# Optimization experiments

Hardware: AMD Instinct MI355X
Metric: run time of the kernel (lower is better)

Reference implementation:

```python
import jax, jax.numpy as jnp
import numpy as np

N_NODES = 100000
N_EDGES = 1600000
D = 32
K = 3  # Chebyshev kernels
NEG_SLOPE = 0.2


def setup_inputs() -> dict:
    key = jax.random.key(0)
    ks = jax.random.split(key, 10)
    s = 1.0 / np.sqrt(D)
    return {
        "u": jax.random.normal(ks[0], (N_NODES, D), jnp.float32),
        "lambda_max": jnp.full((1,), 2.0, jnp.float32),
        "edge_src": jax.random.randint(ks[1], (N_EDGES,), 0, N_NODES, jnp.int32),
        "edge_dst": jax.random.randint(ks[2], (N_EDGES,), 0, N_NODES, jnp.int32),
        "cheb_W": jax.random.normal(ks[3], (K * D, D), jnp.float32) * s,
        "cheb_b": jnp.zeros((D,), jnp.float32),
        "src_W": jax.random.normal(ks[4], (D, D), jnp.float32) * s,
        "src_b": jnp.zeros((D,), jnp.float32),
        "dst_W": jax.random.normal(ks[5], (D, D), jnp.float32) * s,
        "dst_b": jnp.zeros((D,), jnp.float32),
        "attn": jax.random.normal(ks[6], (1, D), jnp.float32) * s,  # (heads=1, D)
    }


def reference(u, lambda_max, edge_src, edge_dst, cheb_W, cheb_b,
              src_W, src_b, dst_W, dst_b, attn):
    N = u.shape[0]
    # in-degrees (DGL: clamp(min=1) ** -0.5)
    deg = jnp.zeros((N,), u.dtype).at[edge_dst].add(1.0)
    Dinv = jnp.clip(deg, 1.0, None) ** -0.5  # (N,)

    def unnL(x):  # D^{-1/2} A D^{-1/2} x  via copy_u->sum message passing
        m = (x * Dinv[:, None])[edge_src]                       # (E, D)
        agg = jax.ops.segment_sum(m, edge_dst, num_segments=N)  # (N, D)
        return agg * Dinv[:, None]

    # --- ChebConv ---
    re_norm = 2.0 / lambda_max  # (1,) broadcast over all nodes
    X0 = u
    Xt = [X0]
    X1 = X0
    if K > 1:
        h = unnL(X0)
        X1 = -re_norm * h + X0 * (re_norm - 1.0)
        Xt.append(X1)
    for _ in range(2, K):
        h = unnL(X1)
        Xi = -2.0 * re_norm * h + X1 * (2.0 * (re_norm - 1.0)) - X0
        Xt.append(Xi)
        X0, X1 = X1, Xi
    Xcat = jnp.concatenate(Xt, axis=1)                 # (N, K*D)
    hc = jax.nn.relu(Xcat @ cheb_W + cheb_b)           # (N, D), DGL default activation=relu

    # --- GATv2Conv (heads=1) ---
    H = attn.shape[0]
    fsrc = (hc @ src_W + src_b).reshape(N, H, -1)      # (N, H, D)
    fdst = (hc @ dst_W + dst_b).reshape(N, H, -1)
    e = jax.nn.leaky_relu(fsrc[edge_src] + fdst[edge_dst], NEG_SLOPE)  # (E, H, D)
    logits = jnp.einsum('ehd,hd->eh', e, attn)         # (E, H)
    mx = jax.ops.segment_max(logits, edge_dst, num_segments=N)
    mx = jnp.where(jnp.isfinite(mx), mx, 0.0)
    ex = jnp.exp(logits - mx[edge_dst])
    den = jax.ops.segment_sum(ex, edge_dst, num_segments=N)
    a = ex / jnp.where(den > 0, den, 1.0)[edge_dst]    # edge softmax over dst groups
    msg = fsrc[edge_src] * a[:, :, None]               # (E, H, D)
    out = jax.ops.segment_sum(msg, edge_dst, num_segments=N)  # (N, H, D)
    return out.squeeze(1)
```

## Files before the change

kernel.cpp:

```cpp
#include <hip/hip_runtime.h>
#include <hip/hip_bf16.h>


typedef unsigned short u16;

#define DD 32
#define NEG_SLOPE 0.2f
#define BLK 256
#define TILE 4096
#define CB_SHIFT 8
#define CB_NODES 256
#define SRC_BITS 17

#define OFF_CHEBW 0
#define OFF_CHEBB 3072
#define OFF_SRCW  3104
#define OFF_SRCB  4128
#define OFF_DSTW  4160
#define OFF_DSTB  5184
#define OFF_ATTN  5216
#define OFF_LMAX  5248
#define W_TOTAL   5249

#define F_U     0
#define F_CHEBW 1
#define F_CHEBB 2
#define F_SRCW  3
#define F_SRCB  4
#define F_DSTW  5
#define F_DSTB  6
#define F_ATTN  7
#define F_LMAX  8
#define N_FLAGS 9

__device__ __forceinline__ float bh2f(u16 h) {
    return __uint_as_float(((unsigned)h) << 16);
}
__device__ __forceinline__ float rdin(const void* p, long long i, int f32f) {
    return f32f ? ((const float*)p)[i] : bh2f(((const u16*)p)[i]);
}
__device__ __forceinline__ float4 rd4(const void* p, long long row, int q, int f32f) {
    if (f32f) return ((const float4*)p)[row * 8 + q];
    ushort4 h = ((const ushort4*)p)[row * 8 + q];
    return make_float4(bh2f(h.x), bh2f(h.y), bh2f(h.z), bh2f(h.w));
}
__device__ __forceinline__ float lrelu(float x) { return fmaxf(x, NEG_SLOPE * x); }

__device__ __forceinline__ int plaus(u16 h) {
    if ((h & 0x7FFFu) == 0) return 1;
    unsigned e = (h >> 7) & 0xFF;
    return (e >= 0x60 && e <= 0x8F) ? 1 : 0;
}

__global__ void k_detect(const void* p0, const void* p1, const void* p2,
                         const void* p3, const void* p4, const void* p5,
                         const void* p6, const void* p7, const void* p8,
                         int n0, int n7, int* __restrict__ flags) {
    __shared__ int cEven, cEvenZ, cOddNZ;
    const void* ptrs[N_FLAGS] = {p0, p1, p2, p3, p4, p5, p6, p7, p8};
    const int   ns[N_FLAGS]   = {n0, 3072, 32, 1024, 32, 1024, 32, n7, 1};
    int a = blockIdx.x;
    if (a >= N_FLAGS) return;
    const u16* h = (const u16*)ptrs[a];
    int n = ns[a];
    if (threadIdx.x == 0) { cEven = 0; cEvenZ = 0; cOddNZ = 0; }
    __syncthreads();
    if (n == 1) {
        if (threadIdx.x == 0) {
            u16 v = h[0];
            flags[a] = ((v & 0x7FFFu) == 0 || !plaus(v)) ? 1 : 0;
        }
        return;
    }
    int nprobe = n >> 1;
    if (nprobe > 64) nprobe = 64;
    int t = threadIdx.x;
    if (t < nprobe) {
        u16 ev = h[2 * t];
        u16 od = h[2 * t + 1];
        if (plaus(ev)) atomicAdd(&cEven, 1);
        if ((ev & 0x7FFFu) == 0) atomicAdd(&cEvenZ, 1);
        if (plaus(od) && (od & 0x7FFFu) != 0) atomicAdd(&cOddNZ, 1);
    }
    __syncthreads();
    if (threadIdx.x == 0) {
        int bf = (cEven * 4 >= nprobe * 3);
        if (cEvenZ == nprobe && cOddNZ * 2 >= nprobe) bf = 0;
        flags[a] = bf ? 0 : 1;
    }
}

__global__ void k_cvtw(const void* chebW, const void* chebB, const void* srcW,
                       const void* srcB, const void* dstW, const void* dstB,
                       const void* attn, const void* lmax,
                       const int* __restrict__ flags, float* __restrict__ wsW,
                       unsigned* __restrict__ Mabs) {
    int i = blockIdx.x * blockDim.x + threadIdx.x;
    if (i >= W_TOTAL + 32) return;
    if (i >= W_TOTAL) { Mabs[i - W_TOTAL] = 0u; return; }
    float v;
    if      (i < OFF_CHEBB) v = rdin(chebW, i - OFF_CHEBW, flags[F_CHEBW]);
    else if (i < OFF_SRCW)  v = rdin(chebB, i - OFF_CHEBB, flags[F_CHEBB]);
    else if (i < OFF_SRCB)  v = rdin(srcW,  i - OFF_SRCW,  flags[F_SRCW]);
    else if (i < OFF_DSTW)  v = rdin(srcB,  i - OFF_SRCB,  flags[F_SRCB]);
    else if (i < OFF_DSTB)  v = rdin(dstW,  i - OFF_DSTW,  flags[F_DSTW]);
    else if (i < OFF_ATTN)  v = rdin(dstB,  i - OFF_DSTB,  flags[F_DSTB]);
    else if (i < OFF_LMAX)  v = rdin(attn,  i - OFF_ATTN,  flags[F_ATTN]);
    else                    v = rdin(lmax,  0,             flags[F_LMAX]);
    wsW[i] = v;
}


__global__ __launch_bounds__(BLK) void k_h1(
        const int* __restrict__ dst, unsigned* __restrict__ hist1,
        int E, int T, int NB1) {
    __shared__ unsigned lh[512];
    int tile = blockIdx.x, t = threadIdx.x;
    for (int b = t; b < 512; b += BLK) lh[b] = 0;
    __syncthreads();
    int base = tile * TILE;
    for (int i = 0; i < TILE / BLK; i++) {
        int e = base + i * BLK + t;
        if (e < E) atomicAdd(&lh[dst[e] >> CB_SHIFT], 1u);
    }
    __syncthreads();
    for (int b = t; b < NB1; b += BLK) hist1[(size_t)b * T + tile] = lh[b];
}

__global__ __launch_bounds__(BLK) void k_scA(
        unsigned* __restrict__ h, unsigned* __restrict__ bsum, int T) {
    __shared__ unsigned s[BLK];
    int b = blockIdx.x, t = threadIdx.x;
    unsigned carry = 0;
    for (int base = 0; base < T; base += BLK) {
        int i = base + t;
        unsigned v = (i < T) ? h[(size_t)b * T + i] : 0u;
        s[t] = v;
        __syncthreads();
        for (int off = 1; off < BLK; off <<= 1) {
            unsigned a = (t >= off) ? s[t - off] : 0u;
            __syncthreads();
            s[t] += a;
            __syncthreads();
        }
        if (i < T) h[(size_t)b * T + i] = carry + s[t] - v;
        carry += s[BLK - 1];
        __syncthreads();
    }
    if (t == 0) bsum[b] = carry;
}

__global__ __launch_bounds__(512) void k_scB(
        unsigned* __restrict__ bsum, int NB1,
        unsigned* __restrict__ row_ptr, int N, int E) {
    __shared__ unsigned s[512];
    int t = threadIdx.x;
    unsigned v = (t < NB1) ? bsum[t] : 0u;
    s[t] = v;
    __syncthreads();
    for (int off = 1; off < 512; off <<= 1) {
        unsigned a = (t >= off) ? s[t - off] : 0u;
        __syncthreads();
        s[t] += a;
        __syncthreads();
    }
    if (t < NB1) bsum[t] = s[t] - v;
    if (t == 0) row_ptr[N] = (unsigned)E;
}

__global__ __launch_bounds__(BLK) void k_s1(
        const int* __restrict__ src, const int* __restrict__ dst,
        const unsigned* __restrict__ off1, const unsigned* __restrict__ bsum,
        unsigned* __restrict__ tmp, int E, int T, int NB1) {
    __shared__ unsigned cur[512];
    int tile = blockIdx.x, t = threadIdx.x;
    for (int b = t; b < NB1; b += BLK)
        cur[b] = off1[(size_t)b * T + tile] + bsum[b];
    __syncthreads();
    int base = tile * TILE;
    for (int i = 0; i < TILE / BLK; i++) {
        int e = base + i * BLK + t;
        if (e < E) {
            int d = dst[e];
            unsigned pos = atomicAdd(&cur[d >> CB_SHIFT], 1u);
            tmp[pos] = ((unsigned)(d & (CB_NODES - 1)) << SRC_BITS) | (unsigned)src[e];
        }
    }
}

__global__ __launch_bounds__(BLK) void k_p2(
        const unsigned* __restrict__ tmp, const unsigned* __restrict__ bsum,
        unsigned* __restrict__ row_ptr, float* __restrict__ dinv,
        int* __restrict__ srcs, int N, int E, int T, int NB1) {
    __shared__ unsigned hist[CB_NODES], cur[CB_NODES], ssc[BLK];
    int b = blockIdx.x, t = threadIdx.x;
    int nodeBase = b << CB_SHIFT;
    unsigned lo = bsum[b];
    unsigned hi = (b + 1 < NB1) ? bsum[b + 1] : (unsigned)E;
    hist[t] = 0;
    __syncthreads();
    for (unsigned e = lo + t; e < hi; e += BLK)
        atomicAdd(&hist[tmp[e] >> SRC_BITS], 1u);
    __syncthreads();
    unsigned v = hist[t];
    ssc[t] = v;
    __syncthreads();
    for (int off = 1; off < BLK; off <<= 1) {
        unsigned a = (t >= off) ? ssc[t - off] : 0u;
        __syncthreads();
        ssc[t] += a;
        __syncthreads();
    }
    unsigned ex = ssc[t] - v;
    cur[t] = ex;
    int node = nodeBase + t;
    if (node < N) {
        row_ptr[node] = lo + ex;
        unsigned c = v;
        if (c < 1u) c = 1u;
        dinv[node] = rsqrtf((float)c);
    }
    __syncthreads();
    for (unsigned e = lo + t; e < hi; e += BLK) {
        unsigned p = tmp[e];
        unsigned pos = lo + atomicAdd(&cur[p >> SRC_BITS], 1u);
        srcs[pos] = (int)(p & ((1u << SRC_BITS) - 1u));
    }
}


__global__ __launch_bounds__(BLK) void k_unnl1(
        const void* __restrict__ u, const int* __restrict__ flags,
        const float* __restrict__ dinv, const unsigned* __restrict__ row_ptr,
        const int* __restrict__ srcs, const float* __restrict__ wsW,
        float* __restrict__ X1, int N) {
    int node = (blockIdx.x * BLK + threadIdx.x) >> 3;
    if (node >= N) return;
    int q = threadIdx.x & 7;
    int f = flags[F_U];
    int base = (int)row_ptr[node], end = (int)row_ptr[node + 1];
    float4 acc = make_float4(0.f, 0.f, 0.f, 0.f);
    for (int i = base; i < end; i += 4) {
        int e1 = i + 1, e2 = i + 2, e3 = i + 3;
        int s0 = srcs[i];
        int s1 = srcs[min(e1, end - 1)];
        int s2 = srcs[min(e2, end - 1)];
        int s3 = srcs[min(e3, end - 1)];
        float dv0 = dinv[s0], dv1 = dinv[s1], dv2 = dinv[s2], dv3 = dinv[s3];
        if (e1 >= end) dv1 = 0.f;
        if (e2 >= end) dv2 = 0.f;
        if (e3 >= end) dv3 = 0.f;
        float4 x0 = rd4(u, s0, q, f);
        float4 x1 = rd4(u, s1, q, f);
        float4 x2 = rd4(u, s2, q, f);
        float4 x3 = rd4(u, s3, q, f);
        acc.x += x0.x * dv0 + x1.x * dv1 + x2.x * dv2 + x3.x * dv3;
        acc.y += x0.y * dv0 + x1.y * dv1 + x2.y * dv2 + x3.y * dv3;
        acc.z += x0.z * dv0 + x1.z * dv1 + x2.z * dv2 + x3.z * dv3;
        acc.w += x0.w * dv0 + x1.w * dv1 + x2.w * dv2 + x3.w * dv3;
    }
    float rn = 2.0f / wsW[OFF_LMAX];
    float dn = dinv[node];
    float4 x0 = rd4(u, node, q, f);
    float4 r;
    r.x = -rn * (acc.x * dn) + x0.x * (rn - 1.f);
    r.y = -rn * (acc.y * dn) + x0.y * (rn - 1.f);
    r.z = -rn * (acc.z * dn) + x0.z * (rn - 1.f);
    r.w = -rn * (acc.w * dn) + x0.w * (rn - 1.f);
    ((float4*)X1)[(size_t)node * 8 + q] = r;
}

__global__ __launch_bounds__(BLK) void k_unnl2(
        const void* __restrict__ u, const int* __restrict__ flags,
        const float* __restrict__ X1, const float* __restrict__ dinv,
        const unsigned* __restrict__ row_ptr, const int* __restrict__ srcs,
        const float* __restrict__ wsW, float* __restrict__ X2, int N) {
    int node = (blockIdx.x * BLK + threadIdx.x) >> 3;
    if (node >= N) return;
    int q = threadIdx.x & 7;
    int base = (int)row_ptr[node], end = (int)row_ptr[node + 1];
    float4 acc = make_float4(0.f, 0.f, 0.f, 0.f);
    for (int i = base; i < end; i += 4) {
        int e1 = i + 1, e2 = i + 2, e3 = i + 3;
        int s0 = srcs[i];
        int s1 = srcs[min(e1, end - 1)];
        int s2 = srcs[min(e2, end - 1)];
        int s3 = srcs[min(e3, end - 1)];
        float dv0 = dinv[s0], dv1 = dinv[s1], dv2 = dinv[s2], dv3 = dinv[s3];
        if (e1 >= end) dv1 = 0.f;
        if (e2 >= end) dv2 = 0.f;
        if (e3 >= end) dv3 = 0.f;
        float4 x0 = ((const float4*)X1)[(size_t)s0 * 8 + q];
        float4 x1 = ((const float4*)X1)[(size_t)s1 * 8 + q];
        float4 x2 = ((const float4*)X1)[(size_t)s2 * 8 + q];
        float4 x3 = ((const float4*)X1)[(size_t)s3 * 8 + q];
        acc.x += x0.x * dv0 + x1.x * dv1 + x2.x * dv2 + x3.x * dv3;
        acc.y += x0.y * dv0 + x1.y * dv1 + x2.y * dv2 + x3.y * dv3;
        acc.z += x0.z * dv0 + x1.z * dv1 + x2.z * dv2 + x3.z * dv3;
        acc.w += x0.w * dv0 + x1.w * dv1 + x2.w * dv2 + x3.w * dv3;
    }
    float rn = 2.0f / wsW[OFF_LMAX];
    float dn = dinv[node];
    float4 x0 = rd4(u, node, q, flags[F_U]);
    float4 x1 = ((const float4*)X1)[(size_t)node * 8 + q];
    float4 r;
    r.x = -2.f * rn * (acc.x * dn) + x1.x * (2.f * (rn - 1.f)) - x0.x;
    r.y = -2.f * rn * (acc.y * dn) + x1.y * (2.f * (rn - 1.f)) - x0.y;
    r.z = -2.f * rn * (acc.z * dn) + x1.z * (2.f * (rn - 1.f)) - x0.z;
    r.w = -2.f * rn * (acc.w * dn) + x1.w * (2.f * (rn - 1.f)) - x0.w;
    ((float4*)X2)[(size_t)node * 8 + q] = r;
}

__global__ __launch_bounds__(BLK) void k_cfsd(
        const void* __restrict__ u, const int* __restrict__ flags,
        const float* __restrict__ X1, const float* __restrict__ X2,
        const float* __restrict__ wsW, float* __restrict__ fsrc,
        float* __restrict__ fdst, unsigned* __restrict__ Mabs, int N) {
    __shared__ float sW[3072], sWs[1024], sWd[1024];
    __shared__ float sb[32], sbs[32], sbd[32];
    __shared__ float hcS[BLK * 33];
    __shared__ unsigned mloc[32];
    int t = threadIdx.x;
    for (int i = t; i < 3072; i += BLK) sW[i] = wsW[OFF_CHEBW + i];
    for (int i = t; i < 1024; i += BLK) {
        sWs[i] = wsW[OFF_SRCW + i];
        sWd[i] = wsW[OFF_DSTW + i];
    }
    if (t < 32) {
        sb[t]  = wsW[OFF_CHEBB + t];
        sbs[t] = wsW[OFF_SRCB + t];
        sbd[t] = wsW[OFF_DSTB + t];
        mloc[t] = 0u;
    }
    __syncthreads();
    int f = flags[F_U];
    float mabs = 0.f;
    int n = blockIdx.x * BLK + t;
    if (n < N) {
        long long row = (long long)n;
        float acc[32];
#pragma unroll
        for (int j = 0; j < 32; j++) acc[j] = sb[j];
        for (int i4 = 0; i4 < 8; i4++) {
            float4 x = rd4(u, row, i4, f);
            const float* w = &sW[i4 * 128];
#pragma unroll
            for (int j = 0; j < 32; j++) acc[j] = fmaf(x.x, w[j], acc[j]);
#pragma unroll
            for (int j = 0; j < 32; j++) acc[j] = fmaf(x.y, w[32 + j], acc[j]);
#pragma unroll
            for (int j = 0; j < 32; j++) acc[j] = fmaf(x.z, w[64 + j], acc[j]);
#pragma unroll
            for (int j = 0; j < 32; j++) acc[j] = fmaf(x.w, w[96 + j], acc[j]);
        }
        for (int i4 = 0; i4 < 8; i4++) {
            float4 x = ((const float4*)X1)[row * 8 + i4];
            const float* w = &sW[1024 + i4 * 128];
#pragma unroll
            for (int j = 0; j < 32; j++) acc[j] = fmaf(x.x, w[j], acc[j]);
#pragma unroll
            for (int j = 0; j < 32; j++) acc[j] = fmaf(x.y, w[32 + j], acc[j]);
#pragma unroll
            for (int j = 0; j < 32; j++) acc[j] = fmaf(x.z, w[64 + j], acc[j]);
#pragma unroll
            for (int j = 0; j < 32; j++) acc[j] = fmaf(x.w, w[96 + j], acc[j]);
        }
        for (int i4 = 0; i4 < 8; i4++) {
            float4 x = ((const float4*)X2)[row * 8 + i4];
            const float* w = &sW[2048 + i4 * 128];
#pragma unroll
            for (int j = 0; j < 32; j++) acc[j] = fmaf(x.x, w[j], acc[j]);
#pragma unroll
            for (int j = 0; j < 32; j++) acc[j] = fmaf(x.y, w[32 + j], acc[j]);
#pragma unroll
            for (int j = 0; j < 32; j++) acc[j] = fmaf(x.z, w[64 + j], acc[j]);
#pragma unroll
            for (int j = 0; j < 32; j++) acc[j] = fmaf(x.w, w[96 + j], acc[j]);
        }
#pragma unroll
        for (int j = 0; j < 32; j++) hcS[t * 33 + j] = fmaxf(acc[j], 0.f);
        float as[32], ad[32];
#pragma unroll
        for (int j = 0; j < 32; j++) { as[j] = sbs[j]; ad[j] = sbd[j]; }
        for (int i = 0; i < 32; i++) {
            float hv = hcS[t * 33 + i];
            const float* ws = &sWs[i * 32];
            const float* wd = &sWd[i * 32];
#pragma unroll
            for (int j = 0; j < 32; j++) {
                as[j] = fmaf(hv, ws[j], as[j]);
                ad[j] = fmaf(hv, wd[j], ad[j]);
            }
        }
        float4* fs4 = (float4*)(fsrc + row * 32);
        float4* fd4 = (float4*)(fdst + row * 32);
#pragma unroll
        for (int i4 = 0; i4 < 8; i4++) {
            fs4[i4] = make_float4(as[4 * i4], as[4 * i4 + 1], as[4 * i4 + 2], as[4 * i4 + 3]);
            fd4[i4] = make_float4(ad[4 * i4], ad[4 * i4 + 1], ad[4 * i4 + 2], ad[4 * i4 + 3]);
        }
#pragma unroll
        for (int j = 0; j < 32; j++) mabs = fmaxf(mabs, fabsf(as[j]));
    }
    atomicMax(&mloc[t & 31], __float_as_uint(mabs));
    __syncthreads();
    if (t < 32) atomicMax(&Mabs[t], mloc[t]);
}

__global__ __launch_bounds__(BLK) void k_gat(
        const float* __restrict__ fsrc, const float* __restrict__ fdst,
        const unsigned* __restrict__ row_ptr, const int* __restrict__ srcs,
        const float* __restrict__ wsW, const unsigned* __restrict__ Mabs,
        float* __restrict__ out, int N) {
    int node = (blockIdx.x * BLK + threadIdx.x) >> 3;
    if (node >= N) return;
    int q = threadIdx.x & 7;
    int base = (int)row_ptr[node], end = (int)row_ptr[node + 1];
    if (base == end) {
        ((float4*)out)[(size_t)node * 8 + q] = make_float4(0.f, 0.f, 0.f, 0.f);
        return;
    }
    float4 fd = ((const float4*)fdst)[(size_t)node * 8 + q];
    float4 at = ((const float4*)(wsW + OFF_ATTN))[q];
    float4 mb = ((const float4*)Mabs)[q];
    float kp = (mb.x + fabsf(fd.x)) * fabsf(at.x) +
               (mb.y + fabsf(fd.y)) * fabsf(at.y) +
               (mb.z + fabsf(fd.z)) * fabsf(at.z) +
               (mb.w + fabsf(fd.w)) * fabsf(at.w);
    kp += __shfl_xor(kp, 1);
    kp += __shfl_xor(kp, 2);
    kp += __shfl_xor(kp, 4);
    float K = kp;
    float4 acc = make_float4(0.f, 0.f, 0.f, 0.f);
    float den = 0.f;
    for (int i = base; i < end; i += 2) {
        int e1 = i + 1;
        int s0 = srcs[i];
        int s1 = srcs[min(e1, end - 1)];
        float4 fs0 = ((const float4*)fsrc)[(size_t)s0 * 8 + q];
        float4 fs1 = ((const float4*)fsrc)[(size_t)s1 * 8 + q];
        float v0 = lrelu(fs0.x + fd.x) * at.x + lrelu(fs0.y + fd.y) * at.y +
                   lrelu(fs0.z + fd.z) * at.z + lrelu(fs0.w + fd.w) * at.w;
        float v1 = lrelu(fs1.x + fd.x) * at.x + lrelu(fs1.y + fd.y) * at.y +
                   lrelu(fs1.z + fd.z) * at.z + lrelu(fs1.w + fd.w) * at.w;
        v0 += __shfl_xor(v0, 1);  v1 += __shfl_xor(v1, 1);
        v0 += __shfl_xor(v0, 2);  v1 += __shfl_xor(v1, 2);
        v0 += __shfl_xor(v0, 4);  v1 += __shfl_xor(v1, 4);
        float w0 = __expf(v0 - K);
        float w1 = (e1 < end) ? __expf(v1 - K) : 0.f;
        acc.x += fs0.x * w0 + fs1.x * w1;
        acc.y += fs0.y * w0 + fs1.y * w1;
        acc.z += fs0.z * w0 + fs1.z * w1;
        acc.w += fs0.w * w0 + fs1.w * w1;
        den += w0 + w1;
    }
    float inv = 1.f / (den > 0.f ? den : 1.f);
    ((float4*)out)[(size_t)node * 8 + q] =
        make_float4(acc.x * inv, acc.y * inv, acc.z * inv, acc.w * inv);
}

extern "C" void kernel_launch(void* const* d_in, const int* in_sizes, int n_in,
                              void* d_out, int out_size, void* d_ws, size_t ws_size,
                              hipStream_t stream) {
    const void* u     = d_in[0];
    const void* lmax  = d_in[1];
    const int*  esrc  = (const int*)d_in[2];
    const int*  edst  = (const int*)d_in[3];
    const void* chebW = d_in[4];
    const void* chebB = d_in[5];
    const void* srcW  = d_in[6];
    const void* srcB  = d_in[7];
    const void* dstW  = d_in[8];
    const void* dstB  = d_in[9];
    const void* attn  = d_in[10];

    const int ND = in_sizes[0];
    const int N  = ND / DD;
    const int E  = in_sizes[2];

    const int NB1 = (N + CB_NODES - 1) >> CB_SHIFT;
    const int T   = (E + TILE - 1) / TILE;
    const int M   = NB1 * T;

    float* ws   = (float*)d_ws;
    float* X1   = ws;
    float* X2   = ws + (size_t)ND;
    unsigned* tmp = (unsigned*)(ws + 2 * (size_t)ND);
    int*   srcs = (int*)(tmp + E);
    unsigned* hist1   = (unsigned*)(srcs + E);
    unsigned* row_ptr = hist1 + M;
    float*    dinv    = (float*)(row_ptr + (N + 1));
    unsigned* bsum    = (unsigned*)(dinv + N);
    float*    wsW     = (float*)(((uintptr_t)(bsum + NB1) + 15) & ~(uintptr_t)15);
    int*      flags   = (int*)(wsW + W_TOTAL);
    unsigned* Mabs    = (unsigned*)(((uintptr_t)(flags + N_FLAGS) + 15) & ~(uintptr_t)15);
    float*    out     = (float*)d_out;

    auto gb = [](long long n, int b) { return (unsigned)((n + b - 1) / b); };

    k_detect<<<N_FLAGS, 64, 0, stream>>>(u, chebW, chebB, srcW, srcB, dstW, dstB,
                                         attn, lmax, ND, DD, flags);
    k_cvtw<<<gb(W_TOTAL + 32, BLK), BLK, 0, stream>>>(chebW, chebB, srcW, srcB,
                                                      dstW, dstB, attn, lmax,
                                                      flags, wsW, Mabs);

    k_h1<<<T, BLK, 0, stream>>>(edst, hist1, E, T, NB1);
    k_scA<<<NB1, BLK, 0, stream>>>(hist1, bsum, T);
    k_scB<<<1, 512, 0, stream>>>(bsum, NB1, row_ptr, N, E);
    k_s1<<<T, BLK, 0, stream>>>(esrc, edst, hist1, bsum, tmp, E, T, NB1);
    k_p2<<<NB1, BLK, 0, stream>>>(tmp, bsum, row_ptr, dinv, srcs, N, E, T, NB1);

    k_unnl1<<<gb((long long)N * 8, BLK), BLK, 0, stream>>>(u, flags, dinv, row_ptr,
                                                           srcs, wsW, X1, N);
    k_unnl2<<<gb((long long)N * 8, BLK), BLK, 0, stream>>>(u, flags, X1, dinv, row_ptr,
                                                           srcs, wsW, X2, N);

    k_cfsd<<<gb(N, BLK), BLK, 0, stream>>>(u, flags, X1, X2, wsW, X1, X2, Mabs, N);

    k_gat<<<gb((long long)N * 8, BLK), BLK, 0, stream>>>(X1, X2, row_ptr, srcs,
                                                         wsW, Mabs, out, N);
}
```

Before: 270.9 us.

## Merge prep kernels, fold bucket scan via last-block, keep hc in registers

Fuses dtype detection and weight conversion into one kernel, so each block converts its own parameter tensor after deciding its format. The second-level bucket scan moves into the last finishing block of k_scA, signalled by a global atomic counter, which removes the k_scB launch. In k_cfsd the relu'd Chebyshev output stays in registers instead of going through a large shared buffer, freeing LDS but raising register pressure. The total number of launches drops by two.

```diff
diff --git a/kernel.cpp b/kernel.cpp
--- a/kernel.cpp
+++ b/kernel.cpp
@@ -52,62 +52,59 @@
     return (e >= 0x60 && e <= 0x8F) ? 1 : 0;
 }
 
-__global__ void k_detect(const void* p0, const void* p1, const void* p2,
-                         const void* p3, const void* p4, const void* p5,
-                         const void* p6, const void* p7, const void* p8,
-                         int n0, int n7, int* __restrict__ flags) {
-    __shared__ int cEven, cEvenZ, cOddNZ;
-    const void* ptrs[N_FLAGS] = {p0, p1, p2, p3, p4, p5, p6, p7, p8};
+__global__ __launch_bounds__(BLK) void k_prep(
+        const void* u, const void* chebW, const void* chebB, const void* srcW,
+        const void* srcB, const void* dstW, const void* dstB, const void* attn,
+        const void* lmax, int n0, int n7, int* __restrict__ flags,
+        float* __restrict__ wsW, unsigned* __restrict__ Mabs,
+        unsigned* __restrict__ gcnt) {
+    __shared__ int cEven, cEvenZ, cOddNZ, fl;
+    const void* ptrs[N_FLAGS] = {u, chebW, chebB, srcW, srcB, dstW, dstB, attn, lmax};
     const int   ns[N_FLAGS]   = {n0, 3072, 32, 1024, 32, 1024, 32, n7, 1};
+    const int   offs[N_FLAGS] = {0, OFF_CHEBW, OFF_CHEBB, OFF_SRCW, OFF_SRCB,
+                                 OFF_DSTW, OFF_DSTB, OFF_ATTN, OFF_LMAX};
     int a = blockIdx.x;
     if (a >= N_FLAGS) return;
+    int t = threadIdx.x;
     const u16* h = (const u16*)ptrs[a];
     int n = ns[a];
-    if (threadIdx.x == 0) { cEven = 0; cEvenZ = 0; cOddNZ = 0; }
+    if (t == 0) { cEven = 0; cEvenZ = 0; cOddNZ = 0; }
+    if (a == 0) {
+        if (t < 32) Mabs[t] = 0u;
+        if (t == 32) *gcnt = 0u;
+    }
     __syncthreads();
     if (n == 1) {
-        if (threadIdx.x == 0) {
+        if (t == 0) {
             u16 v = h[0];
-            flags[a] = ((v & 0x7FFFu) == 0 || !plaus(v)) ? 1 : 0;
-        }
-        return;
-    }
-    int nprobe = n >> 1;
-    if (nprobe > 64) nprobe = 64;
-    int t = threadIdx.x;
-    if (t < nprobe) {
-        u16 ev = h[2 * t];
-        u16 od = h[2 * t + 1];
-        if (plaus(ev)) atomicAdd(&cEven, 1);
-        if ((ev & 0x7FFFu) == 0) atomicAdd(&cEvenZ, 1);
-        if (plaus(od) && (od & 0x7FFFu) != 0) atomicAdd(&cOddNZ, 1);
-    }
-    __syncthreads();
-    if (threadIdx.x == 0) {
-        int bf = (cEven * 4 >= nprobe * 3);
-        if (cEvenZ == nprobe && cOddNZ * 2 >= nprobe) bf = 0;
-        flags[a] = bf ? 0 : 1;
-    }
-}
-
-__global__ void k_cvtw(const void* chebW, const void* chebB, const void* srcW,
-                       const void* srcB, const void* dstW, const void* dstB,
-                       const void* attn, const void* lmax,
-                       const int* __restrict__ flags, float* __restrict__ wsW,
-                       unsigned* __restrict__ Mabs) {
-    int i = blockIdx.x * blockDim.x + threadIdx.x;
-    if (i >= W_TOTAL + 32) return;
-    if (i >= W_TOTAL) { Mabs[i - W_TOTAL] = 0u; return; }
-    float v;
-    if      (i < OFF_CHEBB) v = rdin(chebW, i - OFF_CHEBW, flags[F_CHEBW]);
-    else if (i < OFF_SRCW)  v = rdin(chebB, i - OFF_CHEBB, flags[F_CHEBB]);
-    else if (i < OFF_SRCB)  v = rdin(srcW,  i - OFF_SRCW,  flags[F_SRCW]);
-    else if (i < OFF_DSTW)  v = rdin(srcB,  i - OFF_SRCB,  flags[F_SRCB]);
-    else if (i < OFF_DSTB)  v = rdin(dstW,  i - OFF_DSTW,  flags[F_DSTW]);
-    else if (i < OFF_ATTN)  v = rdin(dstB,  i - OFF_DSTB,  flags[F_DSTB]);
-    else if (i < OFF_LMAX)  v = rdin(attn,  i - OFF_ATTN,  flags[F_ATTN]);
-    else                    v = rdin(lmax,  0,             flags[F_LMAX]);
-    wsW[i] = v;
+            fl = ((v & 0x7FFFu) == 0 || !plaus(v)) ? 1 : 0;
+            flags[a] = fl;
+        }
+    } else {
+        int nprobe = n >> 1;
+        if (nprobe > 64) nprobe = 64;
+        if (t < nprobe) {
+            u16 ev = h[2 * t];
+            u16 od = h[2 * t + 1];
+            if (plaus(ev)) atomicAdd(&cEven, 1);
+            if ((ev & 0x7FFFu) == 0) atomicAdd(&cEvenZ, 1);
+            if (plaus(od) && (od & 0x7FFFu) != 0) atomicAdd(&cOddNZ, 1);
+        }
+        __syncthreads();
+        if (t == 0) {
+            int bf = (cEven * 4 >= nprobe * 3);
+            if (cEvenZ == nprobe && cOddNZ * 2 >= nprobe) bf = 0;
+            fl = bf ? 0 : 1;
+            flags[a] = fl;
+        }
+    }
+    __syncthreads();
+    if (a == 0) return;
+    int f = fl;
+    int cnt = ns[a];
+    int doff = offs[a];
+    for (int i = t; i < cnt; i += BLK)
+        wsW[doff + i] = rdin(ptrs[a], i, f);
 }
 
 
@@ -128,9 +125,13 @@
 }
 
 __global__ __launch_bounds__(BLK) void k_scA(
-        unsigned* __restrict__ h, unsigned* __restrict__ bsum, int T) {
+        unsigned* __restrict__ h, unsigned* __restrict__ bsum, int T,
+        unsigned* __restrict__ row_ptr, int N, int E,
+        unsigned* __restrict__ gcnt) {
     __shared__ unsigned s[BLK];
+    __shared__ int lastdone;
     int b = blockIdx.x, t = threadIdx.x;
+    int NB = gridDim.x;
     unsigned carry = 0;
     for (int base = 0; base < T; base += BLK) {
         int i = base + t;
@@ -147,24 +148,31 @@
         carry += s[BLK - 1];
         __syncthreads();
     }
-    if (t == 0) bsum[b] = carry;
-}
-
-__global__ __launch_bounds__(512) void k_scB(
-        unsigned* __restrict__ bsum, int NB1,
-        unsigned* __restrict__ row_ptr, int N, int E) {
-    __shared__ unsigned s[512];
-    int t = threadIdx.x;
-    unsigned v = (t < NB1) ? bsum[t] : 0u;
-    s[t] = v;
-    __syncthreads();
-    for (int off = 1; off < 512; off <<= 1) {
-        unsigned a = (t >= off) ? s[t - off] : 0u;
-        __syncthreads();
-        s[t] += a;
-        __syncthreads();
-    }
-    if (t < NB1) bsum[t] = s[t] - v;
+    if (t == 0) {
+        bsum[b] = carry;
+        __threadfence();
+        unsigned old = atomicAdd(gcnt, 1u);
+        lastdone = (old == (unsigned)(NB - 1)) ? 1 : 0;
+    }
+    __syncthreads();
+    if (!lastdone) return;
+    __threadfence();
+    unsigned c2 = 0;
+    for (int base = 0; base < NB; base += BLK) {
+        int i = base + t;
+        unsigned v = (i < NB) ? bsum[i] : 0u;
+        s[t] = v;
+        __syncthreads();
+        for (int off = 1; off < BLK; off <<= 1) {
+            unsigned a = (t >= off) ? s[t - off] : 0u;
+            __syncthreads();
+            s[t] += a;
+            __syncthreads();
+        }
+        if (i < NB) bsum[i] = c2 + s[t] - v;
+        c2 += s[BLK - 1];
+        __syncthreads();
+    }
     if (t == 0) row_ptr[N] = (unsigned)E;
 }
 
@@ -318,7 +326,6 @@
         float* __restrict__ fdst, unsigned* __restrict__ Mabs, int N) {
     __shared__ float sW[3072], sWs[1024], sWd[1024];
     __shared__ float sb[32], sbs[32], sbd[32];
-    __shared__ float hcS[BLK * 33];
     __shared__ unsigned mloc[32];
     int t = threadIdx.x;
     for (int i = t; i < 3072; i += BLK) sW[i] = wsW[OFF_CHEBW + i];
@@ -378,12 +385,13 @@
             for (int j = 0; j < 32; j++) acc[j] = fmaf(x.w, w[96 + j], acc[j]);
         }
 #pragma unroll
-        for (int j = 0; j < 32; j++) hcS[t * 33 + j] = fmaxf(acc[j], 0.f);
+        for (int j = 0; j < 32; j++) acc[j] = fmaxf(acc[j], 0.f);
         float as[32], ad[32];
 #pragma unroll
         for (int j = 0; j < 32; j++) { as[j] = sbs[j]; ad[j] = sbd[j]; }
+#pragma unroll
         for (int i = 0; i < 32; i++) {
-            float hv = hcS[t * 33 + i];
+            float hv = acc[i];
             const float* ws = &sWs[i * 32];
             const float* wd = &sWd[i * 32];
 #pragma unroll
@@ -494,19 +502,16 @@
     float*    wsW     = (float*)(((uintptr_t)(bsum + NB1) + 15) & ~(uintptr_t)15);
     int*      flags   = (int*)(wsW + W_TOTAL);
     unsigned* Mabs    = (unsigned*)(((uintptr_t)(flags + N_FLAGS) + 15) & ~(uintptr_t)15);
+    unsigned* gcnt    = Mabs + 32;
     float*    out     = (float*)d_out;
 
     auto gb = [](long long n, int b) { return (unsigned)((n + b - 1) / b); };
 
-    k_detect<<<N_FLAGS, 64, 0, stream>>>(u, chebW, chebB, srcW, srcB, dstW, dstB,
-                                         attn, lmax, ND, DD, flags);
-    k_cvtw<<<gb(W_TOTAL + 32, BLK), BLK, 0, stream>>>(chebW, chebB, srcW, srcB,
-                                                      dstW, dstB, attn, lmax,
-                                                      flags, wsW, Mabs);
+    k_prep<<<N_FLAGS, BLK, 0, stream>>>(u, chebW, chebB, srcW, srcB, dstW, dstB,
+                                        attn, lmax, ND, DD, flags, wsW, Mabs, gcnt);
 
     k_h1<<<T, BLK, 0, stream>>>(edst, hist1, E, T, NB1);
-    k_scA<<<NB1, BLK, 0, stream>>>(hist1, bsum, T);
-    k_scB<<<1, 512, 0, stream>>>(bsum, NB1, row_ptr, N, E);
+    k_scA<<<NB1, BLK, 0, stream>>>(hist1, bsum, T, row_ptr, N, E, gcnt);
     k_s1<<<T, BLK, 0, stream>>>(esrc, edst, hist1, bsum, tmp, E, T, NB1);
     k_p2<<<NB1, BLK, 0, stream>>>(tmp, bsum, row_ptr, dinv, srcs, N, E, T, NB1);
 
```

Result: slower. 278.5 us (+2.8%).
